# Kernel tuning notes

Hardware: AMD Instinct MI355X
Metric: run time of the kernel (lower is better)

The kernel has to match this reference:

```python
import jax, jax.numpy as jnp
import numpy as np

# ---- static frequency grid from init kwargs ----
POS_FREQS = 31
W_MIN, W_MAX = 0.1, 1.0
PATCH = 16

def _build_grid():
    g = (W_MAX / W_MIN) ** (1.0 / (POS_FREQS - 1))
    pos_w = (W_MIN * g ** np.arange(POS_FREQS)).astype(np.float32)
    Wx = np.concatenate([-pos_w[::-1], [0.0], pos_w]).astype(np.float32)  # len 63
    Wy = np.concatenate([[0.0], pos_w]).astype(np.float32)               # len 32
    pad_h = (PATCH - len(Wx) % PATCH) % PATCH  # 1 -> H=64
    pad_w = (PATCH - len(Wy) % PATCH) % PATCH  # 0 -> W=32
    U, V = np.meshgrid(Wx, Wy, indexing='ij')
    U = np.pad(U, ((0, pad_h), (0, pad_w))).astype(np.float32)
    V = np.pad(V, ((0, pad_h), (0, pad_w))).astype(np.float32)
    pad_mask = np.ones_like(U)
    if pad_h > 0:
        pad_mask[-pad_h:, :] = 0.0
    if pad_w > 0:
        pad_mask[:, -pad_w:] = 0.0
    return U, V, pad_mask

_U, _V, _PADMASK = _build_grid()
H, W = _U.shape


def _cft_triangles(tris):
    """Closed-form CFT of each triangle over the HxW frequency grid.
    tris: [T,3,2] float32 -> [T,H,W] complex64."""
    pi = np.float32(np.pi)
    U = jnp.asarray(_U)[None]  # [1,H,W]
    V = jnp.asarray(_V)[None]
    xq = tris[:, 0, 0][:, None, None]; yq = tris[:, 0, 1][:, None, None]
    xr = tris[:, 1, 0][:, None, None]; yr = tris[:, 1, 1][:, None, None]
    xs = tris[:, 2, 0][:, None, None]; ys = tris[:, 2, 1][:, None, None]
    det = xq * (yr - ys) + xr * (ys - yq) + xs * (yq - yr)
    area = jnp.abs(0.5 * det)  # [T,1,1]
    U_ = U * (xr - xq) + V * (yr - yq)  # [T,H,W]
    V_ = U * (xs - xr) + V * (ys - yr)
    phase_shift = jnp.exp(-2j * pi * (U * xq + V * yq))
    zero_mask = (U_ == 0) & (V_ == 0)
    diag_mask = (U_ + V_ == 0) & ~zero_mask
    u_mask = (U_ == 0) & ~zero_mask
    v_mask = (V_ == 0) & ~zero_mask
    normal_mask = ~(diag_mask | zero_mask | u_mask | v_mask)
    four_pi2 = np.float32(4.0) * pi * pi

    def inv_safe(den, m):
        # masked reciprocal with safe denominator (keeps grads finite)
        return jnp.where(m, 1.0, 0.0) / jnp.where(m, den, 1.0)

    part1 = (inv_safe(four_pi2 * U_ * V_ * (U_ + V_), normal_mask)
             - inv_safe(four_pi2 * U_ * U_, diag_mask)
             - inv_safe(four_pi2 * V_ * V_, u_mask)
             + inv_safe(four_pi2 * U_ * U_, v_mask))
    base_u = jnp.exp(-2j * pi * U_)
    base_v = jnp.exp(-2j * pi * V_)
    base_uv = jnp.exp(-2j * pi * (U_ + V_))
    j2pi = 2j * pi
    part2 = (jnp.where(normal_mask, -U_ * base_uv + (U_ + V_) * base_u - V_, 0.0)
             + jnp.where(diag_mask, base_u + j2pi * U_ - 1.0, 0.0)
             + jnp.where(u_mask, base_v + j2pi * V_ - 1.0, 0.0)
             + jnp.where(v_mask, (j2pi * U_ + 1.0) * base_u - 1.0, 0.0))
    FT = 2.0 * area * part1 * part2 * phase_shift
    FT = jnp.where(zero_mask, area.astype(jnp.complex64), FT)
    return FT * jnp.asarray(_PADMASK)[None]


def _forward(batch_triangles, lengths):
    B, maxN = batch_triangles.shape[:2]
    FT = _cft_triangles(batch_triangles.reshape(B * maxN, 3, 2))
    FT = FT.reshape(B, maxN, H, W)
    valid = (jnp.arange(maxN)[None, :] < lengths[:, None]).astype(jnp.float32)
    FT_total = jnp.sum(FT * valid[:, :, None, None], axis=1)  # segment-sum by polygon
    re, im = FT_total.real, FT_total.imag
    m2 = re * re + im * im
    is0 = m2 == 0
    mag = jnp.where(is0, 0.0, jnp.sqrt(jnp.where(is0, 1.0, m2)))
    phase = jnp.arctan2(im, jnp.where(is0, 1.0, re))  # angle(0)=0 like torch
    mag = jnp.log1p(mag)
    return mag[:, None], phase[:, None]  # [B,1,H,W] each


def setup_inputs() -> dict:
    key = jax.random.key(0)
    k1, k2 = jax.random.split(key)
    batch_triangles = jax.random.normal(k1, (64, 128, 3, 2), dtype=jnp.float32)
    lengths = jax.random.randint(k2, (64,), 0, 128, dtype=jnp.int32)
    return {"batch_triangles": batch_triangles, "lengths": lengths}


def reference(batch_triangles, lengths):
    return _forward(batch_triangles, lengths)
```

## Files before the change

kernel.cpp:

```cpp
#include <hip/hip_runtime.h>
#include <cmath>

#define BB     64
#define MAXN   128
#define HH     64
#define WW     32
#define NFREQ  (HH*WW)
#define BLK    256
#define PCHUNKS (NFREQ/BLK)
#define TRI_CHUNK 16
#define QQ     (MAXN/TRI_CHUNK)

__device__ __forceinline__ void sincos_2pi(float x, float* s, float* c) {
    float r = __builtin_amdgcn_fractf(x);
    *s = __builtin_amdgcn_sinf(r);
    *c = __builtin_amdgcn_cosf(r);
}

__device__ __forceinline__ void eval_tri(
    float U, float V, float4 A4, float4 B4, float& accR, float& accI,
    float TWOPI, float FOUR_PI2)
{
    const float xq = A4.x,  yq = A4.y,  e1x = A4.z, e1y = A4.w;
    const float e2x = B4.x, e2y = B4.y, area = B4.z;

    const float U_ = __fadd_rn(__fmul_rn(U, e1x), __fmul_rn(V, e1y));
    const float V_ = __fadd_rn(__fmul_rn(U, e2x), __fmul_rn(V, e2y));
    const float S  = __fadd_rn(U_, V_);

    const bool uz   = (U_ == 0.0f);
    const bool vz   = (V_ == 0.0f);
    const bool sz   = (S  == 0.0f);
    const bool zero = uz && vz;
    const bool diag = sz && !zero;
    const bool u_m  = uz && !zero;
    const bool v_m  = vz && !zero;
    const bool nrm  = !(uz || vz || sz);

    const float t_q = U * xq + V * yq;
    const float t_r = t_q + U_;
    const float t_s = t_r + V_;

    float s_q, c_q, s_r, c_r, s_s, c_s;
    sincos_2pi(t_q, &s_q, &c_q);
    sincos_2pi(t_r, &s_r, &c_r);
    sincos_2pi(t_s, &s_s, &c_s);

    const float twU = TWOPI * U_;
    const float twV = TWOPI * V_;

    const float Ac = nrm ? -U_ : (u_m ? 1.0f : 0.0f);
    const float Bc = nrm ?  S  : ((diag || v_m) ? 1.0f : 0.0f);
    const float Cc = nrm ? -V_ : -1.0f;
    const float Dc = v_m  ? twU : 0.0f;
    const float Ec = diag ? twU : (u_m ? twV : 0.0f);

    const float d1  = u_m ? V_ : U_;
    const float den = nrm ? (U_ * V_) * S : d1 * d1;
    const float p1  = __builtin_amdgcn_rcpf(FOUR_PI2 * den);
    const float sgn = (diag || u_m) ? -2.0f : 2.0f;
    const float k   = zero ? 0.0f : sgn * area * p1;

    const float re =  Ac * c_s + Bc * c_r + Cc * c_q + Dc * s_r + Ec * s_q;
    const float im = -(Ac * s_s + Bc * s_r + Cc * s_q) + Dc * c_r + Ec * c_q;

    accR = fmaf(k, re, accR) + (zero ? area : 0.0f);
    accI = fmaf(k, im, accI);
}

__global__ __launch_bounds__(BLK) void poly_cft_partial(
    const float* __restrict__ tris,
    const int*   __restrict__ lengths,
    float2*      __restrict__ ws)
{
    __shared__ float4 sA[TRI_CHUNK];
    __shared__ float4 sB[TRI_CHUNK];
    __shared__ float  s_posw[31];

    const int pc = blockIdx.x;
    const int q  = blockIdx.y;
    const int b  = blockIdx.z;
    const int p  = (pc << 8) | threadIdx.x;
    const int h  = p >> 5;
    const int w  = p & 31;

    const int N   = lengths[b];
    const int n0  = q * TRI_CHUNK;
    const int cnt = min(n0 + TRI_CHUNK, N) - n0;

    if (cnt <= 0) return;

    if (threadIdx.x < 31) {
        double g = pow(10.0, 1.0 / 30.0);
        s_posw[threadIdx.x] = (float)(0.1 * pow(g, (double)threadIdx.x));
    }

    if (threadIdx.x < TRI_CHUNK) {
        if ((int)threadIdx.x < cnt) {
            const float* t = tris + ((size_t)b * MAXN + n0 + threadIdx.x) * 6;
            float xq = t[0], yq = t[1];
            float xr = t[2], yr = t[3];
            float xs = t[4], ys = t[5];
            float det  = xq * (yr - ys) + xr * (ys - yq) + xs * (yq - yr);
            float area = fabsf(0.5f * det);
            sA[threadIdx.x] = make_float4(xq, yq, xr - xq, yr - yq);
            sB[threadIdx.x] = make_float4(xs - xr, ys - yr, area, 0.0f);
        } else {
            sA[threadIdx.x] = make_float4(0.0f, 0.0f, 0.0f, 0.0f);
            sB[threadIdx.x] = make_float4(0.0f, 0.0f, 0.0f, 0.0f);
        }
    }
    __syncthreads();

    float U;
    if (h < 31)       U = -s_posw[30 - h];
    else if (h == 31) U = 0.0f;
    else if (h < 63)  U = s_posw[h - 32];
    else              U = 0.0f;
    const float V = (w == 0) ? 0.0f : s_posw[w - 1];

    const float PI_F     = 3.14159274101257324f;
    const float TWOPI    = 6.28318548202514648f;
    const float FOUR_PI2 = (4.0f * PI_F) * PI_F;

    float accR = 0.0f, accI = 0.0f;

#pragma unroll 4
    for (int n = 0; n < TRI_CHUNK; ++n) {
        eval_tri(U, V, sA[n], sB[n], accR, accI, TWOPI, FOUR_PI2);
    }

    ws[((size_t)q * BB + b) * NFREQ + p] = make_float2(accR, accI);
}

__global__ __launch_bounds__(BLK) void poly_cft_finalize(
    const float2* __restrict__ ws,
    const int*    __restrict__ lengths,
    float*        __restrict__ out)
{
    const int idx = blockIdx.x * BLK + threadIdx.x;
    const int b = idx >> 11;
    const int p = idx & (NFREQ - 1);
    const int h = p >> 5;

    const int QN = (lengths[b] + TRI_CHUNK - 1) / TRI_CHUNK;

    float accR = 0.0f, accI = 0.0f;
    for (int q = 0; q < QN; ++q) {
        float2 v = ws[((size_t)q * BB + b) * NFREQ + p];
        accR += v.x;
        accI += v.y;
    }

    if (h == 63) { accR = 0.0f; accI = 0.0f; }

    const float m2 = __fadd_rn(__fmul_rn(accR, accR), __fmul_rn(accI, accI));
    float mag, ph;
    if (m2 == 0.0f) {
        mag = 0.0f;
        ph  = atan2f(accI, 1.0f);
    } else {
        mag = log1pf(sqrtf(m2));
        ph  = atan2f(accI, accR);
    }

    out[idx]              = mag;
    out[BB * NFREQ + idx] = ph;
}

extern "C" void kernel_launch(void* const* d_in, const int* in_sizes, int n_in,
                              void* d_out, int out_size, void* d_ws, size_t ws_size,
                              hipStream_t stream) {
    const float* tris    = (const float*)d_in[0];
    const int*   lengths = (const int*)d_in[1];
    float*       out     = (float*)d_out;
    float2*      partial = (float2*)d_ws;

    poly_cft_partial<<<dim3(PCHUNKS, QQ, BB), dim3(BLK), 0, stream>>>(tris, lengths, partial);
    poly_cft_finalize<<<dim3(BB * NFREQ / BLK), dim3(BLK), 0, stream>>>(partial, lengths, out);
}
```

Before: 79.17 us.

## Fuse partial and finalize kernels with in-block wave reduction over triangles

Replaces the two-kernel scheme (partial sums per triangle chunk written to workspace, then a finalize pass) with a single kernel. Each block covers 64 frequencies for one polygon, and its four waves split the triangles round-robin. Triangle data is loaded as wave-uniform scalar loads, and the waves combine their sums through shared memory before computing magnitude and phase. This removes the workspace round trip and the second launch. In exchange, per-polygon work is no longer split across chunk blocks, so load balance now depends on each polygon's triangle count.

```diff
diff --git a/kernel.cpp b/kernel.cpp
--- a/kernel.cpp
+++ b/kernel.cpp
@@ -7,9 +7,8 @@
 #define WW     32
 #define NFREQ  (HH*WW)
 #define BLK    256
-#define PCHUNKS (NFREQ/BLK)
-#define TRI_CHUNK 16
-#define QQ     (MAXN/TRI_CHUNK)
+#define NWAVE  4
+#define PGRPS  (NFREQ/64)
 
 __device__ __forceinline__ void sincos_2pi(float x, float* s, float* c) {
     float r = __builtin_amdgcn_fractf(x);
@@ -68,47 +67,25 @@
     accI = fmaf(k, im, accI);
 }
 
-__global__ __launch_bounds__(BLK) void poly_cft_partial(
+__global__ __launch_bounds__(BLK) void poly_cft_fused(
     const float* __restrict__ tris,
     const int*   __restrict__ lengths,
-    float2*      __restrict__ ws)
+    float*       __restrict__ out)
 {
-    __shared__ float4 sA[TRI_CHUNK];
-    __shared__ float4 sB[TRI_CHUNK];
     __shared__ float  s_posw[31];
+    __shared__ float2 s_red[NWAVE][64];
 
-    const int pc = blockIdx.x;
-    const int q  = blockIdx.y;
-    const int b  = blockIdx.z;
-    const int p  = (pc << 8) | threadIdx.x;
-    const int h  = p >> 5;
-    const int w  = p & 31;
-
-    const int N   = lengths[b];
-    const int n0  = q * TRI_CHUNK;
-    const int cnt = min(n0 + TRI_CHUNK, N) - n0;
-
-    if (cnt <= 0) return;
+    const int pg   = blockIdx.x;
+    const int b    = blockIdx.y;
+    const int lane = threadIdx.x & 63;
+    const int wv   = threadIdx.x >> 6;
+    const int p    = (pg << 6) | lane;
+    const int h    = p >> 5;
+    const int w    = p & 31;
 
     if (threadIdx.x < 31) {
         double g = pow(10.0, 1.0 / 30.0);
         s_posw[threadIdx.x] = (float)(0.1 * pow(g, (double)threadIdx.x));
-    }
-
-    if (threadIdx.x < TRI_CHUNK) {
-        if ((int)threadIdx.x < cnt) {
-            const float* t = tris + ((size_t)b * MAXN + n0 + threadIdx.x) * 6;
-            float xq = t[0], yq = t[1];
-            float xr = t[2], yr = t[3];
-            float xs = t[4], ys = t[5];
-            float det  = xq * (yr - ys) + xr * (ys - yq) + xs * (yq - yr);
-            float area = fabsf(0.5f * det);
-            sA[threadIdx.x] = make_float4(xq, yq, xr - xq, yr - yq);
-            sB[threadIdx.x] = make_float4(xs - xr, ys - yr, area, 0.0f);
-        } else {
-            sA[threadIdx.x] = make_float4(0.0f, 0.0f, 0.0f, 0.0f);
-            sB[threadIdx.x] = make_float4(0.0f, 0.0f, 0.0f, 0.0f);
-        }
     }
     __syncthreads();
 
@@ -123,49 +100,55 @@
     const float TWOPI    = 6.28318548202514648f;
     const float FOUR_PI2 = (4.0f * PI_F) * PI_F;
 
+    const int N = lengths[b];
+    const float* __restrict__ tb = tris + (size_t)b * MAXN * 6;
+
     float accR = 0.0f, accI = 0.0f;
 
-#pragma unroll 4
-    for (int n = 0; n < TRI_CHUNK; ++n) {
-        eval_tri(U, V, sA[n], sB[n], accR, accI, TWOPI, FOUR_PI2);
+#pragma unroll 2
+    for (int n = wv; n < N; n += NWAVE) {
+        const int nn = __builtin_amdgcn_readfirstlane(n);
+        const float* t = tb + nn * 6;
+        const float xq = t[0], yq = t[1];
+        const float xr = t[2], yr = t[3];
+        const float xs = t[4], ys = t[5];
+        const float det  = xq * (yr - ys) + xr * (ys - yq) + xs * (yq - yr);
+        const float area = fabsf(0.5f * det);
+        const float4 A4 = make_float4(xq, yq, xr - xq, yr - yq);
+        const float4 B4 = make_float4(xs - xr, ys - yr, area, 0.0f);
+        eval_tri(U, V, A4, B4, accR, accI, TWOPI, FOUR_PI2);
     }
 
-    ws[((size_t)q * BB + b) * NFREQ + p] = make_float2(accR, accI);
-}
+    s_red[wv][lane] = make_float2(accR, accI);
+    __syncthreads();
 
-__global__ __launch_bounds__(BLK) void poly_cft_finalize(
-    const float2* __restrict__ ws,
-    const int*    __restrict__ lengths,
-    float*        __restrict__ out)
-{
-    const int idx = blockIdx.x * BLK + threadIdx.x;
-    const int b = idx >> 11;
-    const int p = idx & (NFREQ - 1);
-    const int h = p >> 5;
+    if (wv == 0) {
+        float R = 0.0f, I = 0.0f;
+#pragma unroll
+        for (int k = 0; k < NWAVE; ++k) {
+            const float2 v = s_red[k][lane];
+            R += v.x;
+            I += v.y;
+        }
+        R += 0.0f;
+        I += 0.0f;
 
-    const int QN = (lengths[b] + TRI_CHUNK - 1) / TRI_CHUNK;
+        if (h == 63) { R = 0.0f; I = 0.0f; }
 
-    float accR = 0.0f, accI = 0.0f;
-    for (int q = 0; q < QN; ++q) {
-        float2 v = ws[((size_t)q * BB + b) * NFREQ + p];
-        accR += v.x;
-        accI += v.y;
+        const float m2 = __fadd_rn(__fmul_rn(R, R), __fmul_rn(I, I));
+        float mag, ph;
+        if (m2 == 0.0f) {
+            mag = 0.0f;
+            ph  = atan2f(I, 1.0f);
+        } else {
+            mag = log1pf(sqrtf(m2));
+            ph  = atan2f(I, R);
+        }
+
+        const int o = b * NFREQ + p;
+        out[o]              = mag;
+        out[BB * NFREQ + o] = ph;
     }
-
-    if (h == 63) { accR = 0.0f; accI = 0.0f; }
-
-    const float m2 = __fadd_rn(__fmul_rn(accR, accR), __fmul_rn(accI, accI));
-    float mag, ph;
-    if (m2 == 0.0f) {
-        mag = 0.0f;
-        ph  = atan2f(accI, 1.0f);
-    } else {
-        mag = log1pf(sqrtf(m2));
-        ph  = atan2f(accI, accR);
-    }
-
-    out[idx]              = mag;
-    out[BB * NFREQ + idx] = ph;
 }
 
 extern "C" void kernel_launch(void* const* d_in, const int* in_sizes, int n_in,
@@ -174,8 +157,6 @@
     const float* tris    = (const float*)d_in[0];
     const int*   lengths = (const int*)d_in[1];
     float*       out     = (float*)d_out;
-    float2*      partial = (float2*)d_ws;
 
-    poly_cft_partial<<<dim3(PCHUNKS, QQ, BB), dim3(BLK), 0, stream>>>(tris, lengths, partial);
-    poly_cft_finalize<<<dim3(BB * NFREQ / BLK), dim3(BLK), 0, stream>>>(partial, lengths, out);
+    poly_cft_fused<<<dim3(PGRPS, BB), dim3(BLK), 0, stream>>>(tris, lengths, out);
 }
```

New measurement: 76.95 us. 2.8% less time.
